# Kernel tuning notes

Hardware: AMD Instinct MI355X
Metric: run time of the kernel (lower is better)

## Reference

```python
import jax, jax.numpy as jnp
import numpy as np
import math

N = 4096; NFEAT = 512; HID = 128; H = 4; DH = HID // H; NC = 16; FF = 2 * HID


def _ln(x, g, b):
    m = jnp.mean(x, -1, keepdims=True)
    v = jnp.var(x, -1, keepdims=True)
    return (x - m) / jnp.sqrt(v + 1e-5) * g + b


def setup_inputs() -> dict:
    key = jax.random.key(0)
    ks = jax.random.split(key, 16)

    def w(k, shape):
        s = 1.0 / np.sqrt(shape[0])
        return jax.random.uniform(k, shape, jnp.float32, -s, s)

    inp = {}
    inp['e'] = jax.random.uniform(ks[0], (N,), jnp.float32, 0.0, 2.0)  # eigenvalues
    inp['u'] = jax.random.normal(ks[1], (N, N), jnp.float32) / np.sqrt(N)  # eigenvectors
    inp['x'] = jax.random.normal(ks[2], (N, NFEAT), jnp.float32)
    # feat_encoder: Linear(nfeat,hid) -> ReLU -> Linear(hid,nclass)
    inp['fe_w1'] = w(ks[3], (NFEAT, HID)); inp['fe_b1'] = jnp.zeros((HID,), jnp.float32)
    inp['fe_w2'] = w(ks[4], (HID, NC));    inp['fe_b2'] = jnp.zeros((NC,), jnp.float32)
    # eig_w: Linear(hid+1, hid)
    inp['ew_w'] = w(ks[5], (HID + 1, HID)); inp['ew_b'] = jnp.zeros((HID,), jnp.float32)
    inp['ln1_g'] = jnp.ones((HID,), jnp.float32); inp['ln1_b'] = jnp.zeros((HID,), jnp.float32)
    # custom MHA projections
    inp['wq'] = w(ks[6], (HID, HID)); inp['bq'] = jnp.zeros((HID,), jnp.float32)
    inp['wk'] = w(ks[7], (HID, HID)); inp['bk'] = jnp.zeros((HID,), jnp.float32)
    inp['wv'] = w(ks[8], (HID, HID)); inp['bv'] = jnp.zeros((HID,), jnp.float32)
    inp['wo'] = w(ks[9], (HID, HID)); inp['bo'] = jnp.zeros((HID,), jnp.float32)
    inp['ln2_g'] = jnp.ones((HID,), jnp.float32); inp['ln2_b'] = jnp.zeros((HID,), jnp.float32)
    # FFN with GELU
    inp['ffn_w1'] = w(ks[10], (HID, FF)); inp['ffn_b1'] = jnp.zeros((FF,), jnp.float32)
    inp['ffn_w2'] = w(ks[11], (FF, HID)); inp['ffn_b2'] = jnp.zeros((HID,), jnp.float32)
    # decoder: Linear(hid, nheads)
    inp['dec_w'] = w(ks[12], (HID, H)); inp['dec_b'] = jnp.zeros((H,), jnp.float32)
    # SpecLayer weight (norm='none' -> ones, [1, nheads+1, nclass])
    inp['spec_w'] = jnp.ones((1, H + 1, NC), jnp.float32)
    return inp


def reference(e, u, x, fe_w1, fe_b1, fe_w2, fe_b2, ew_w, ew_b, ln1_g, ln1_b,
              wq, bq, wk, bk, wv, bv, wo, bo, ln2_g, ln2_b,
              ffn_w1, ffn_b1, ffn_w2, ffn_b2, dec_w, dec_b, spec_w):
    n = e.shape[0]
    # feat_encoder (norm='none' path), dropout is identity at p=0
    h = jax.nn.relu(x @ fe_w1 + fe_b1) @ fe_w2 + fe_b2  # [N, NC]
    # SineEncoding
    div = jnp.exp(jnp.arange(0, HID, 2, dtype=jnp.float32) * (-math.log(10000.0) / HID))  # [HID/2]
    pe = (e * 100.0)[:, None] * div                     # [N, HID/2]
    sc = jnp.concatenate([jnp.sin(pe), jnp.cos(pe)], axis=1)   # [N, HID] (sin_cos_encoding)
    eeig = jnp.concatenate([e[:, None], sc], axis=1)           # [N, HID+1]
    eigw = eeig @ ew_w + ew_b                                  # [N, HID]
    # Custom multi-head attention with dot-product relative-position bias
    m = _ln(eigw, ln1_g, ln1_b)
    q = (m @ wq + bq).reshape(n, H, DH).transpose(1, 0, 2)     # [H, N, DH]
    k = (m @ wk + bk).reshape(n, H, DH).transpose(1, 0, 2)
    v = (m @ wv + bv).reshape(n, H, DH).transpose(1, 0, 2)
    rel = sc @ sc.T                                            # [N, N]
    scale = 1.0 / math.sqrt(DH)
    scores = jnp.einsum('hnd,hmd->hnm', q, k) * scale + rel[None] * scale  # [H, N, N]
    attn = jax.nn.softmax(scores, axis=-1)
    out = jnp.einsum('hnm,hmd->hnd', attn, v).transpose(1, 0, 2).reshape(n, HID)
    out = out @ wo + bo
    eig = eigw + out
    f = _ln(eig, ln2_g, ln2_b)
    f = jax.nn.gelu(f @ ffn_w1 + ffn_b1, approximate=False) @ ffn_w2 + ffn_b2
    eig = eig + f
    new_e = eig @ dec_w + dec_b                                # [N, H]
    # Spectral propagation (single SpecLayer, norm='none')
    utx = u.T @ h                                              # [N, NC]
    scaled = new_e.T[:, :, None] * utx[None]                   # [H, N, NC]
    props = jnp.einsum('nm,hmc->hnc', u, scaled)               # [H, N, NC]
    bf = jnp.concatenate([h[:, None, :], props.transpose(1, 0, 2)], axis=1)  # [N, H+1, NC]
    return jnp.sum(bf * spec_w, axis=1)                        # [N, NC]
```

## Files before the change

### kernel.cpp

```cpp
#include <hip/hip_runtime.h>
#include <math.h>

#define N 4096
#define NFEAT 512
#define HID 128
#define NHEAD 4
#define DH 32
#define NC 16
#define FF 256
#define NSPLIT 32
#define NCHUNK 8
#define CHUNKM (N / NCHUNK)
#define NGRP (CHUNKM / 128)

typedef _Float16 f16;
typedef unsigned int uint;
typedef _Float16 f16x8 __attribute__((ext_vector_type(8)));
typedef _Float16 f16x2 __attribute__((ext_vector_type(2)));
typedef float f32x16 __attribute__((ext_vector_type(16)));

#define SCALE 0.17677669529663687f
#define LOG2E 1.44269504088896f
#define SH2   (-14.0f * 1.44269504088896f)

__global__ __launch_bounds__(256) void k_feat(const float* __restrict__ x,
    const float* __restrict__ w1, const float* __restrict__ b1,
    const float* __restrict__ w2, const float* __restrict__ b2,
    float* __restrict__ h) {
  __shared__ float xs[8][NFEAT];
  __shared__ float h1s[8][HID];
  int r0 = blockIdx.x * 8, tid = threadIdx.x;
  for (int i = tid; i < 8 * (NFEAT / 4); i += 256) {
    int rr = i >> 7, c4 = i & 127;
    ((float4*)xs[rr])[c4] = *(const float4*)(x + (size_t)(r0 + rr) * NFEAT + c4 * 4);
  }
  __syncthreads();
  int c = tid & 127, rb = tid >> 7;
  float acc[4];
#pragma unroll
  for (int i = 0; i < 4; ++i) acc[i] = b1[c];
  for (int k2 = 0; k2 < NFEAT; ++k2) {
    float wv = w1[k2 * HID + c];
#pragma unroll
    for (int i = 0; i < 4; ++i) acc[i] += xs[rb + 2 * i][k2] * wv;
  }
#pragma unroll
  for (int i = 0; i < 4; ++i) h1s[rb + 2 * i][c] = fmaxf(acc[i], 0.f);
  __syncthreads();
  if (tid < 128) {
    int rr = tid >> 4, cc = tid & 15;
    float a2 = b2[cc];
    for (int k2 = 0; k2 < HID; ++k2)
      a2 += h1s[rr][k2] * w2[k2 * NC + cc];
    h[(size_t)(r0 + rr) * NC + cc] = a2;
  }
}

__global__ __launch_bounds__(256) void k_sine_eigw(const float* __restrict__ e,
    const float* __restrict__ eww, const float* __restrict__ ewb,
    f16* __restrict__ sc_h, f16* __restrict__ scS_h, float* __restrict__ eigw) {
  __shared__ float scs[8][HID];
  __shared__ float es[8];
  int r0 = blockIdx.x * 8, tid = threadIdx.x;
  if (tid < 8) es[tid] = e[r0 + tid];
  __syncthreads();
  for (int i = tid; i < 8 * 64; i += 256) {
    int rr = i >> 6, j = i & 63;
    float div = expf((float)(2 * j) * (-0.07195578415606394f));
    float pe = es[rr] * 100.0f * div;
    scs[rr][j]      = sinf(pe);
    scs[rr][j + 64] = cosf(pe);
  }
  __syncthreads();
  for (int i = tid; i < 8 * 64; i += 256) {
    int rr = i >> 6, jj = i & 63;
    float x0 = scs[rr][2 * jj], x1 = scs[rr][2 * jj + 1];
    f16x2 a; a[0] = (f16)x0; a[1] = (f16)x1;
    f16x2 b; b[0] = (f16)(x0 * SCALE); b[1] = (f16)(x1 * SCALE);
    ((f16x2*)sc_h)[(size_t)(r0 + rr) * 64 + jj] = a;
    ((f16x2*)scS_h)[(size_t)(r0 + rr) * 64 + jj] = b;
  }
  int c = tid & 127, rb = tid >> 7;
  float acc[4];
#pragma unroll
  for (int i = 0; i < 4; ++i) acc[i] = ewb[c] + es[rb + 2 * i] * eww[c];
  for (int k2 = 0; k2 < HID; ++k2) {
    float wv = eww[(1 + k2) * HID + c];
#pragma unroll
    for (int i = 0; i < 4; ++i) acc[i] += scs[rb + 2 * i][k2] * wv;
  }
#pragma unroll
  for (int i = 0; i < 4; ++i)
    eigw[(size_t)(r0 + rb + 2 * i) * HID + c] = acc[i];
}

__global__ __launch_bounds__(256) void k_ln(const float* __restrict__ in,
    const float* __restrict__ g, const float* __restrict__ b, float* __restrict__ out) {
  int row = blockIdx.x * 4 + (threadIdx.x >> 6);
  int l = threadIdx.x & 63;
  float2 v2 = *(const float2*)(in + (size_t)row * HID + l * 2);
  float s = v2.x + v2.y;
  float ss = v2.x * v2.x + v2.y * v2.y;
#pragma unroll
  for (int off = 32; off > 0; off >>= 1) {
    s  += __shfl_down(s, off, 64);
    ss += __shfl_down(ss, off, 64);
  }
  s = __shfl(s, 0, 64); ss = __shfl(ss, 0, 64);
  float mean = s * (1.0f / HID);
  float var = ss * (1.0f / HID) - mean * mean;
  float inv = 1.0f / sqrtf(var + 1e-5f);
  float2 g2 = *(const float2*)(g + l * 2);
  float2 b2 = *(const float2*)(b + l * 2);
  float2 o;
  o.x = (v2.x - mean) * inv * g2.x + b2.x;
  o.y = (v2.y - mean) * inv * g2.y + b2.y;
  *(float2*)(out + (size_t)row * HID + l * 2) = o;
}

template <bool RES, bool F16O>
__global__ __launch_bounds__(256) void k_lin128(const float* __restrict__ in,
    const float* __restrict__ w, const float* __restrict__ bias,
    const float* __restrict__ res, float* __restrict__ out, f16* __restrict__ outh,
    float oscale) {
  __shared__ float as[8][HID];
  int r0 = blockIdx.x * 8, tid = threadIdx.x;
  {
    int rr = tid >> 5, c4 = tid & 31;
    ((float4*)as[rr])[c4] = *(const float4*)(in + (size_t)(r0 + rr) * HID + c4 * 4);
  }
  __syncthreads();
  int c = tid & 127, rb = tid >> 7;
  float acc[4];
#pragma unroll
  for (int i = 0; i < 4; ++i) acc[i] = bias[c];
  for (int k2 = 0; k2 < HID; ++k2) {
    float wv = w[k2 * HID + c];
#pragma unroll
    for (int i = 0; i < 4; ++i) acc[i] += as[rb + 2 * i][k2] * wv;
  }
#pragma unroll
  for (int i = 0; i < 4; ++i) {
    int rr = rb + 2 * i;
    float o = acc[i];
    if (RES) o += res[(size_t)(r0 + rr) * HID + c];
    if (F16O) outh[(size_t)(r0 + rr) * HID + c] = (f16)(o * oscale);
    else      out[(size_t)(r0 + rr) * HID + c] = o;
  }
}

__global__ __launch_bounds__(256) void k_vT(const float* __restrict__ v, f16* __restrict__ vT) {
  int n0 = blockIdx.x * 64, d0 = blockIdx.y * 32, tid = threadIdx.x;
  int d = tid & 31;
#pragma unroll
  for (int it = 0; it < 4; ++it) {
    int j = (tid >> 5) + it * 8;
    float x0 = v[(size_t)(n0 + 2 * j) * HID + d0 + d];
    float x1 = v[(size_t)(n0 + 2 * j + 1) * HID + d0 + d];
    f16x2 hh; hh[0] = (f16)x0; hh[1] = (f16)x1;
    ((f16x2*)vT)[((size_t)(d0 + d) * N + n0) / 2 + j] = hh;
  }
}

__global__ __launch_bounds__(256, 4) void k_attn2(const f16* __restrict__ qh, const f16* __restrict__ kh,
    const f16* __restrict__ vTh, const f16* __restrict__ sch, const f16* __restrict__ scSh,
    float* __restrict__ pacc, float* __restrict__ pl) {
  __shared__ float relbuf[4 * 4 * 64 * 4];
  int tid = threadIdx.x, w = tid >> 6, lane = tid & 63, lrow = lane & 31, lhalf = lane >> 5;
  int n0 = blockIdx.x * 32, ntile = blockIdx.x, chunk = blockIdx.y;
  const f16* qp = qh + (size_t)(n0 + lrow) * HID + 32 * w + lhalf * 8;
  f16x8 qb0 = *(const f16x8*)(qp);
  f16x8 qb1 = *(const f16x8*)(qp + 16);
  f32x16 oacc = {0,0,0,0,0,0,0,0,0,0,0,0,0,0,0,0};
  float l = 0.f;
  for (int g = 0; g < NGRP; ++g) {
    int m0my = chunk * CHUNKM + (g * 4 + w) * 32;
    f32x16 rs = {0,0,0,0,0,0,0,0,0,0,0,0,0,0,0,0};
#pragma unroll
    for (int ks = 0; ks < 8; ++ks) {
      f16x8 as = *(const f16x8*)(scSh + (size_t)(m0my + lrow) * HID + ks * 16 + lhalf * 8);
      f16x8 bs = *(const f16x8*)(sch + (size_t)(n0 + lrow) * HID + ks * 16 + lhalf * 8);
      rs = __builtin_amdgcn_mfma_f32_32x32x16_f16(as, bs, rs, 0, 0, 0);
    }
    __syncthreads();
    {
      int base = w * 1024 + lane * 4;
      *(float4*)&relbuf[base +   0] = make_float4(rs[0],  rs[1],  rs[2],  rs[3]);
      *(float4*)&relbuf[base + 256] = make_float4(rs[4],  rs[5],  rs[6],  rs[7]);
      *(float4*)&relbuf[base + 512] = make_float4(rs[8],  rs[9],  rs[10], rs[11]);
      *(float4*)&relbuf[base + 768] = make_float4(rs[12], rs[13], rs[14], rs[15]);
    }
    __syncthreads();
#pragma unroll
    for (int t = 0; t < 4; ++t) {
      int m0 = chunk * CHUNKM + (g * 4 + t) * 32;
      f32x16 sacc;
      {
        int base = t * 1024 + lane * 4;
        float4 r0 = *(const float4*)&relbuf[base +   0];
        float4 r1 = *(const float4*)&relbuf[base + 256];
        float4 r2 = *(const float4*)&relbuf[base + 512];
        float4 r3 = *(const float4*)&relbuf[base + 768];
        sacc[0]=r0.x;  sacc[1]=r0.y;  sacc[2]=r0.z;  sacc[3]=r0.w;
        sacc[4]=r1.x;  sacc[5]=r1.y;  sacc[6]=r1.z;  sacc[7]=r1.w;
        sacc[8]=r2.x;  sacc[9]=r2.y;  sacc[10]=r2.z; sacc[11]=r2.w;
        sacc[12]=r3.x; sacc[13]=r3.y; sacc[14]=r3.z; sacc[15]=r3.w;
      }
      const f16* kp = kh + (size_t)(m0 + lrow) * HID + 32 * w + lhalf * 8;
      f16x8 ka0 = *(const f16x8*)(kp);
      f16x8 ka1 = *(const f16x8*)(kp + 16);
      const f16* vp = vTh + (size_t)(32 * w + lrow) * N + m0 + lhalf * 8;
      f16x8 va0 = *(const f16x8*)(vp);
      f16x8 va1 = *(const f16x8*)(vp + 16);
      sacc = __builtin_amdgcn_mfma_f32_32x32x16_f16(ka0, qb0, sacc, 0, 0, 0);
      sacc = __builtin_amdgcn_mfma_f32_32x32x16_f16(ka1, qb1, sacc, 0, 0, 0);
      uint w0[2], w1[2], w2[2], w3[2];
#pragma unroll
      for (int ks = 0; ks < 2; ++ks) {
        float p[8];
#pragma unroll
        for (int i = 0; i < 8; ++i)
          p[i] = exp2f(fmaf(sacc[ks * 8 + i], LOG2E, SH2));
        uint Wa = __builtin_bit_cast(uint, __builtin_amdgcn_cvt_pkrtz(p[0], p[1]));
        uint Wb = __builtin_bit_cast(uint, __builtin_amdgcn_cvt_pkrtz(p[2], p[3]));
        uint Wc = __builtin_bit_cast(uint, __builtin_amdgcn_cvt_pkrtz(p[4], p[5]));
        uint Wd = __builtin_bit_cast(uint, __builtin_amdgcn_cvt_pkrtz(p[6], p[7]));
        {
          f16x2 ha = __builtin_bit_cast(f16x2, Wa), hb = __builtin_bit_cast(f16x2, Wb);
          f16x2 hc = __builtin_bit_cast(f16x2, Wc), hd = __builtin_bit_cast(f16x2, Wd);
          l += (float)ha[0] + (float)ha[1] + (float)hb[0] + (float)hb[1]
             + (float)hc[0] + (float)hc[1] + (float)hd[0] + (float)hd[1];
        }
        uint Wax = (uint)__shfl_xor((int)Wa, 32, 64);
        uint Wbx = (uint)__shfl_xor((int)Wb, 32, 64);
        uint Wcx = (uint)__shfl_xor((int)Wc, 32, 64);
        uint Wdx = (uint)__shfl_xor((int)Wd, 32, 64);
        bool hi = (lhalf != 0);
        w0[ks] = hi ? Wcx : Wa;
        w1[ks] = hi ? Wdx : Wb;
        w2[ks] = hi ? Wc : Wax;
        w3[ks] = hi ? Wd : Wbx;
      }
      f16x8 pb0 = __builtin_bit_cast(f16x8, make_uint4(w0[0], w1[0], w2[0], w3[0]));
      f16x8 pb1 = __builtin_bit_cast(f16x8, make_uint4(w0[1], w1[1], w2[1], w3[1]));
      oacc = __builtin_amdgcn_mfma_f32_32x32x16_f16(va0, pb0, oacc, 0, 0, 0);
      oacc = __builtin_amdgcn_mfma_f32_32x32x16_f16(va1, pb1, oacc, 0, 0, 0);
    }
  }
  l += __shfl_xor(l, 32, 64);
  float* pp = pacc + ((size_t)(chunk * 4 + w) * 128 + ntile) * 1024 + lane * 16;
  *(float4*)(pp +  0) = make_float4(oacc[0],  oacc[1],  oacc[2],  oacc[3]);
  *(float4*)(pp +  4) = make_float4(oacc[4],  oacc[5],  oacc[6],  oacc[7]);
  *(float4*)(pp +  8) = make_float4(oacc[8],  oacc[9],  oacc[10], oacc[11]);
  *(float4*)(pp + 12) = make_float4(oacc[12], oacc[13], oacc[14], oacc[15]);
  if (lane < 32) pl[(size_t)(chunk * 4 + w) * N + n0 + lrow] = l;
}

__global__ __launch_bounds__(256) void k_attn_merge2(const float* __restrict__ pacc,
    const float* __restrict__ pl, float* __restrict__ attno) {
  __shared__ float ao[32][132];
  int tid = threadIdx.x, h = tid >> 6, lane = tid & 63, lrow = lane & 31, lhalf = lane >> 5;
  int ntile = blockIdx.x, n0 = ntile * 32;
  float o[16];
#pragma unroll
  for (int r = 0; r < 16; ++r) o[r] = 0.f;
  float l = 0.f;
#pragma unroll
  for (int c = 0; c < NCHUNK; ++c) {
    const float* pp = pacc + ((size_t)(c * 4 + h) * 128 + ntile) * 1024 + lane * 16;
    float4 r0 = *(const float4*)(pp), r1 = *(const float4*)(pp + 4);
    float4 r2 = *(const float4*)(pp + 8), r3 = *(const float4*)(pp + 12);
    o[0]+=r0.x; o[1]+=r0.y; o[2]+=r0.z; o[3]+=r0.w;
    o[4]+=r1.x; o[5]+=r1.y; o[6]+=r1.z; o[7]+=r1.w;
    o[8]+=r2.x; o[9]+=r2.y; o[10]+=r2.z; o[11]+=r2.w;
    o[12]+=r3.x; o[13]+=r3.y; o[14]+=r3.z; o[15]+=r3.w;
    l += pl[(size_t)(c * 4 + h) * N + n0 + lrow];
  }
  float inv = 1.0f / l;
#pragma unroll
  for (int r = 0; r < 16; ++r) {
    int d = (r & 3) + 8 * (r >> 2) + 4 * lhalf;
    ao[lrow][h * 32 + d] = o[r] * inv;
  }
  __syncthreads();
  for (int i = tid; i < 32 * 32; i += 256) {
    int row = i >> 5, c4 = i & 31;
    *(float4*)(attno + (size_t)(n0 + row) * HID + c4 * 4) = *(float4*)&ao[row][c4 * 4];
  }
}

__global__ __launch_bounds__(256) void k_ffn(const float* __restrict__ fln,
    const float* __restrict__ w1, const float* __restrict__ b1,
    const float* __restrict__ w2, const float* __restrict__ b2,
    const float* __restrict__ eig, float* __restrict__ out) {
  __shared__ float fs[8][HID];
  __shared__ float t1[8][FF];
  int r0 = blockIdx.x * 8, tid = threadIdx.x;
  {
    int rr = tid >> 5, c4 = tid & 31;
    ((float4*)fs[rr])[c4] = *(const float4*)(fln + (size_t)(r0 + rr) * HID + c4 * 4);
  }
  __syncthreads();
  {
    float acc[8];
#pragma unroll
    for (int i = 0; i < 8; ++i) acc[i] = b1[tid];
    for (int k2 = 0; k2 < HID; ++k2) {
      float wv = w1[k2 * FF + tid];
#pragma unroll
      for (int i = 0; i < 8; ++i) acc[i] += fs[i][k2] * wv;
    }
#pragma unroll
    for (int i = 0; i < 8; ++i) {
      float xg = acc[i];
      t1[i][tid] = 0.5f * xg * (1.0f + erff(xg * 0.7071067811865476f));
    }
  }
  __syncthreads();
  int c = tid & 127, rb = tid >> 7;
  float acc2[4];
#pragma unroll
  for (int i = 0; i < 4; ++i) acc2[i] = b2[c];
  for (int k2 = 0; k2 < FF; ++k2) {
    float wv = w2[k2 * HID + c];
#pragma unroll
    for (int i = 0; i < 4; ++i) acc2[i] += t1[rb + 2 * i][k2] * wv;
  }
#pragma unroll
  for (int i = 0; i < 4; ++i) {
    int rr = r0 + rb + 2 * i;
    out[(size_t)rr * HID + c] = acc2[i] + eig[(size_t)rr * HID + c];
  }
}

__global__ __launch_bounds__(256) void k_dec(const float* __restrict__ eig2,
    const float* __restrict__ dw, const float* __restrict__ db, float* __restrict__ newe) {
  int tid = threadIdx.x;
  int r = tid >> 4, j = (tid >> 2) & 3, q = tid & 3;
  int n = blockIdx.x * 16 + r;
  const float* ep = eig2 + (size_t)n * HID + q * 32;
  float a = 0.f;
#pragma unroll
  for (int t4 = 0; t4 < 8; ++t4) {
    float4 e4 = *(const float4*)(ep + t4 * 4);
    int k0 = q * 32 + t4 * 4;
    a += e4.x * dw[k0 * NHEAD + j] + e4.y * dw[(k0 + 1) * NHEAD + j]
       + e4.z * dw[(k0 + 2) * NHEAD + j] + e4.w * dw[(k0 + 3) * NHEAD + j];
  }
  a += __shfl_down(a, 1, 64);
  a += __shfl_down(a, 2, 64);
  if (q == 0) newe[n * NHEAD + j] = db[j] + a;
}

__global__ __launch_bounds__(256) void k_utx(const float* __restrict__ u,
    const float* __restrict__ h, float* __restrict__ putx) {
  __shared__ float hs[128][NC];
  int tid = threadIdx.x;
  int m = blockIdx.x * 256 + tid;
  int n0 = blockIdx.y * 128;
  for (int i = tid; i < 128 * 4; i += 256) {
    int row = i >> 2, cq = i & 3;
    ((float4*)hs[row])[cq] = *(const float4*)(h + (size_t)(n0 + row) * NC + cq * 4);
  }
  __syncthreads();
  float acc[16];
#pragma unroll
  for (int c = 0; c < 16; ++c) acc[c] = 0.f;
  for (int nb = 0; nb < 16; ++nb) {
    float uv[8];
#pragma unroll
    for (int t = 0; t < 8; ++t)
      uv[t] = u[(size_t)(n0 + nb * 8 + t) * N + m];
#pragma unroll
    for (int t = 0; t < 8; ++t) {
      int nl = nb * 8 + t;
      float4 h0 = ((const float4*)hs[nl])[0];
      float4 h1 = ((const float4*)hs[nl])[1];
      float4 h2 = ((const float4*)hs[nl])[2];
      float4 h3 = ((const float4*)hs[nl])[3];
      acc[0]  += uv[t] * h0.x;  acc[1]  += uv[t] * h0.y;
      acc[2]  += uv[t] * h0.z;  acc[3]  += uv[t] * h0.w;
      acc[4]  += uv[t] * h1.x;  acc[5]  += uv[t] * h1.y;
      acc[6]  += uv[t] * h1.z;  acc[7]  += uv[t] * h1.w;
      acc[8]  += uv[t] * h2.x;  acc[9]  += uv[t] * h2.y;
      acc[10] += uv[t] * h2.z;  acc[11] += uv[t] * h2.w;
      acc[12] += uv[t] * h3.x;  acc[13] += uv[t] * h3.y;
      acc[14] += uv[t] * h3.z;  acc[15] += uv[t] * h3.w;
    }
  }
  float* o = putx + ((size_t)blockIdx.y * N + m) * NC;
  *(float4*)(o +  0) = make_float4(acc[0],  acc[1],  acc[2],  acc[3]);
  *(float4*)(o +  4) = make_float4(acc[4],  acc[5],  acc[6],  acc[7]);
  *(float4*)(o +  8) = make_float4(acc[8],  acc[9],  acc[10], acc[11]);
  *(float4*)(o + 12) = make_float4(acc[12], acc[13], acc[14], acc[15]);
}

__global__ __launch_bounds__(256) void k_sbuild(const float* __restrict__ putx,
    const float* __restrict__ newe, const float* __restrict__ specw,
    float* __restrict__ sT) {
  int i = blockIdx.x * 256 + threadIdx.x;
  int m = i >> 2, cq = i & 3;
  float4 t = make_float4(0.f, 0.f, 0.f, 0.f);
#pragma unroll 8
  for (int ch = 0; ch < NSPLIT; ++ch) {
    float4 p = *(const float4*)(putx + ((size_t)ch * N + m) * NC + cq * 4);
    t.x += p.x; t.y += p.y; t.z += p.z; t.w += p.w;
  }
  float4 ne = *(const float4*)(newe + (size_t)m * NHEAD);
  float fac[4];
#pragma unroll
  for (int cc = 0; cc < 4; ++cc) {
    int c = cq * 4 + cc;
    fac[cc] = ne.x * specw[1 * NC + c] + ne.y * specw[2 * NC + c]
            + ne.z * specw[3 * NC + c] + ne.w * specw[4 * NC + c];
  }
  sT[(size_t)(cq * 4 + 0) * N + m] = t.x * fac[0];
  sT[(size_t)(cq * 4 + 1) * N + m] = t.y * fac[1];
  sT[(size_t)(cq * 4 + 2) * N + m] = t.z * fac[2];
  sT[(size_t)(cq * 4 + 3) * N + m] = t.w * fac[3];
}

__global__ __launch_bounds__(256) void k_final(const float* __restrict__ u,
    const float* __restrict__ sT, float* __restrict__ pfin) {
  __shared__ float sTl[16][256];
  int tid = threadIdx.x, w = tid >> 6, lane = tid & 63;
  int r0 = blockIdx.x * 16;
  size_t mbase = (size_t)blockIdx.y * 2048;
  float a[4][16];
#pragma unroll
  for (int r = 0; r < 4; ++r)
#pragma unroll
    for (int c = 0; c < 16; ++c) a[r][c] = 0.f;
  for (int chunk = 0; chunk < 8; ++chunk) {
    size_t mc0 = mbase + chunk * 256;
    __syncthreads();
    for (int i = tid; i < 16 * 64; i += 256) {
      int c = i >> 6, q = i & 63;
      ((float4*)&sTl[c][0])[q] = *(const float4*)(sT + (size_t)c * N + mc0 + q * 4);
    }
    __syncthreads();
    float4 u4[4];
#pragma unroll
    for (int r = 0; r < 4; ++r)
      u4[r] = *(const float4*)(u + (size_t)(r0 + w * 4 + r) * N + mc0 + 4 * lane);
#pragma unroll
    for (int c = 0; c < 16; ++c) {
      float4 sv = *(const float4*)&sTl[c][4 * lane];
#pragma unroll
      for (int r = 0; r < 4; ++r)
        a[r][c] += u4[r].x * sv.x + u4[r].y * sv.y + u4[r].z * sv.z + u4[r].w * sv.w;
    }
  }
#pragma unroll
  for (int off = 32; off > 0; off >>= 1)
#pragma unroll
    for (int r = 0; r < 4; ++r)
#pragma unroll
      for (int c = 0; c < 16; ++c)
        a[r][c] += __shfl_xor(a[r][c], off, 64);
  if (lane == 0) {
#pragma unroll
    for (int r = 0; r < 4; ++r) {
      float* op = pfin + ((size_t)blockIdx.y * N + r0 + w * 4 + r) * NC;
      *(float4*)(op +  0) = make_float4(a[r][0],  a[r][1],  a[r][2],  a[r][3]);
      *(float4*)(op +  4) = make_float4(a[r][4],  a[r][5],  a[r][6],  a[r][7]);
      *(float4*)(op +  8) = make_float4(a[r][8],  a[r][9],  a[r][10], a[r][11]);
      *(float4*)(op + 12) = make_float4(a[r][12], a[r][13], a[r][14], a[r][15]);
    }
  }
}

__global__ __launch_bounds__(256) void k_finmerge(const float* __restrict__ pfin,
    const float* __restrict__ h, const float* __restrict__ specw, float* __restrict__ out) {
  int i = blockIdx.x * 256 + threadIdx.x;
  int n = i >> 2, cq = i & 3;
  float4 f0 = *(const float4*)(pfin + (size_t)n * NC + cq * 4);
  float4 f1 = *(const float4*)(pfin + ((size_t)N + n) * NC + cq * 4);
  float4 h4 = *(const float4*)(h + (size_t)n * NC + cq * 4);
  int c0 = cq * 4;
  float4 o;
  o.x = f0.x + f1.x + h4.x * specw[c0 + 0];
  o.y = f0.y + f1.y + h4.y * specw[c0 + 1];
  o.z = f0.z + f1.z + h4.z * specw[c0 + 2];
  o.w = f0.w + f1.w + h4.w * specw[c0 + 3];
  *(float4*)(out + (size_t)n * NC + cq * 4) = o;
}

extern "C" void kernel_launch(void* const* d_in, const int* in_sizes, int n_in,
                              void* d_out, int out_size, void* d_ws, size_t ws_size,
                              hipStream_t stream) {
  const float* e    = (const float*)d_in[0];
  const float* u    = (const float*)d_in[1];
  const float* x    = (const float*)d_in[2];
  const float* few1 = (const float*)d_in[3];
  const float* feb1 = (const float*)d_in[4];
  const float* few2 = (const float*)d_in[5];
  const float* feb2 = (const float*)d_in[6];
  const float* eww  = (const float*)d_in[7];
  const float* ewb  = (const float*)d_in[8];
  const float* ln1g = (const float*)d_in[9];
  const float* ln1b = (const float*)d_in[10];
  const float* wq   = (const float*)d_in[11];
  const float* bq   = (const float*)d_in[12];
  const float* wk   = (const float*)d_in[13];
  const float* bk   = (const float*)d_in[14];
  const float* wv_  = (const float*)d_in[15];
  const float* bv   = (const float*)d_in[16];
  const float* wo   = (const float*)d_in[17];
  const float* bo   = (const float*)d_in[18];
  const float* ln2g = (const float*)d_in[19];
  const float* ln2b = (const float*)d_in[20];
  const float* fw1  = (const float*)d_in[21];
  const float* fb1  = (const float*)d_in[22];
  const float* fw2  = (const float*)d_in[23];
  const float* fb2  = (const float*)d_in[24];
  const float* dw   = (const float*)d_in[25];
  const float* db   = (const float*)d_in[26];
  const float* spw  = (const float*)d_in[27];
  float* out = (float*)d_out;

  char* wsb = (char*)d_ws;
  auto alloc = [&](size_t bytes) { char* p = wsb; wsb += (bytes + 1023) & ~(size_t)1023; return p; };
  float* h    = (float*)alloc(N * NC * 4);
  f16*  sc_h  = (f16*)alloc(N * HID * 2);
  f16*  scS_h = (f16*)alloc(N * HID * 2);
  float* eigw = (float*)alloc(N * HID * 4);
  float* mln  = (float*)alloc(N * HID * 4);
  f16*  q_h   = (f16*)alloc(N * HID * 2);
  f16*  k_h   = (f16*)alloc(N * HID * 2);
  float* v    = (float*)alloc(N * HID * 4);
  f16*  vT_h  = (f16*)alloc(N * HID * 2);
  float* attno= (float*)alloc(N * HID * 4);
  float* eig  = (float*)alloc(N * HID * 4);
  float* fln  = (float*)alloc(N * HID * 4);
  float* eig2 = (float*)alloc(N * HID * 4);
  float* newe = (float*)alloc(N * NHEAD * 4);
  float* sT   = (float*)alloc((size_t)NC * N * 4);
  float* putx = (float*)alloc((size_t)NSPLIT * N * NC * 4);
  float* pacc = (float*)alloc((size_t)NCHUNK * 4 * 128 * 1024 * 4);
  float* pl   = (float*)alloc((size_t)NCHUNK * 4 * N * 4);
  float* pfin = (float*)alloc((size_t)2 * N * NC * 4);

  k_feat<<<N / 8, 256, 0, stream>>>(x, few1, feb1, few2, feb2, h);
  k_utx<<<dim3(N / 256, NSPLIT), 256, 0, stream>>>(u, h, putx);
  k_sine_eigw<<<N / 8, 256, 0, stream>>>(e, eww, ewb, sc_h, scS_h, eigw);
  k_ln<<<N / 4, 256, 0, stream>>>(eigw, ln1g, ln1b, mln);
  k_lin128<false, true><<<N / 8, 256, 0, stream>>>(mln, wq, bq, nullptr, nullptr, q_h, SCALE);
  k_lin128<false, true><<<N / 8, 256, 0, stream>>>(mln, wk, bk, nullptr, nullptr, k_h, 1.0f);
  k_lin128<false, false><<<N / 8, 256, 0, stream>>>(mln, wv_, bv, nullptr, v, nullptr, 1.0f);
  k_vT<<<dim3(N / 64, 4), 256, 0, stream>>>(v, vT_h);
  k_attn2<<<dim3(128, NCHUNK), 256, 0, stream>>>(q_h, k_h, vT_h, sc_h, scS_h, pacc, pl);
  k_attn_merge2<<<128, 256, 0, stream>>>(pacc, pl, attno);
  k_lin128<true, false><<<N / 8, 256, 0, stream>>>(attno, wo, bo, eigw, eig, nullptr, 1.0f);
  k_ln<<<N / 4, 256, 0, stream>>>(eig, ln2g, ln2b, fln);
  k_ffn<<<N / 8, 256, 0, stream>>>(fln, fw1, fb1, fw2, fb2, eig, eig2);
  k_dec<<<N / 16, 256, 0, stream>>>(eig2, dw, db, newe);
  k_sbuild<<<N * 4 / 256, 256, 0, stream>>>(putx, newe, spw, sT);
  k_final<<<dim3(N / 16, 2), 256, 0, stream>>>(u, sT, pfin);
  k_finmerge<<<N * 4 / 256, 256, 0, stream>>>(pfin, h, spw, out);
}
```

Measured before the change: 378.0 us.

## Fuse LayerNorm with QKV projections and split attention into more chunks

Replaces the separate LayerNorm kernel and three linear-projection launches with one kernel that normalizes each row in shared memory and computes Q, K and V together, removing the intermediate buffer and three launches. The attention kernel now splits the key dimension into twice as many chunks and requests higher occupancy, so more blocks run concurrently at the cost of more partial results for the merge step. Inside attention, the softmax denominator is summed in fp32 before conversion to f16, and where available a lane-32 permute swap replaces four cross-half shuffles. The occupancy hint may force register spills, and the larger partial buffer adds merge traffic; the merge kernel must also handle the new chunk count.

```diff
diff --git a/kernel.cpp b/kernel.cpp
--- a/kernel.cpp
+++ b/kernel.cpp
@@ -9,7 +9,7 @@
 #define NC 16
 #define FF 256
 #define NSPLIT 32
-#define NCHUNK 8
+#define NCHUNK 16
 #define CHUNKM (N / NCHUNK)
 #define NGRP (CHUNKM / 128)
 
@@ -18,6 +18,7 @@
 typedef _Float16 f16x8 __attribute__((ext_vector_type(8)));
 typedef _Float16 f16x2 __attribute__((ext_vector_type(2)));
 typedef float f32x16 __attribute__((ext_vector_type(16)));
+typedef uint uint2v __attribute__((ext_vector_type(2)));
 
 #define SCALE 0.17677669529663687f
 #define LOG2E 1.44269504088896f
@@ -118,6 +119,60 @@
   *(float2*)(out + (size_t)row * HID + l * 2) = o;
 }
 
+__global__ __launch_bounds__(256) void k_lnqkv(const float* __restrict__ eigw,
+    const float* __restrict__ g, const float* __restrict__ b,
+    const float* __restrict__ wq, const float* __restrict__ bq,
+    const float* __restrict__ wk, const float* __restrict__ bk,
+    const float* __restrict__ wv, const float* __restrict__ bv,
+    f16* __restrict__ qh, f16* __restrict__ kh, float* __restrict__ v) {
+  __shared__ float as[8][HID];
+  int r0 = blockIdx.x * 8, tid = threadIdx.x;
+  {
+    int rr = tid >> 5, ln = tid & 31;
+    float4 x4 = *(const float4*)(eigw + (size_t)(r0 + rr) * HID + ln * 4);
+    float s = x4.x + x4.y + x4.z + x4.w;
+    float ss = x4.x * x4.x + x4.y * x4.y + x4.z * x4.z + x4.w * x4.w;
+#pragma unroll
+    for (int off = 16; off > 0; off >>= 1) {
+      s  += __shfl_xor(s, off, 32);
+      ss += __shfl_xor(ss, off, 32);
+    }
+    float mean = s * (1.0f / HID);
+    float var = ss * (1.0f / HID) - mean * mean;
+    float inv = 1.0f / sqrtf(var + 1e-5f);
+    float4 g4 = *(const float4*)(g + ln * 4);
+    float4 b4 = *(const float4*)(b + ln * 4);
+    float4 o;
+    o.x = (x4.x - mean) * inv * g4.x + b4.x;
+    o.y = (x4.y - mean) * inv * g4.y + b4.y;
+    o.z = (x4.z - mean) * inv * g4.z + b4.z;
+    o.w = (x4.w - mean) * inv * g4.w + b4.w;
+    *(float4*)&as[rr][ln * 4] = o;
+  }
+  __syncthreads();
+  int c = tid & 127, rb = tid >> 7;
+  float aq[4], ak[4], av[4];
+#pragma unroll
+  for (int i = 0; i < 4; ++i) { aq[i] = bq[c]; ak[i] = bk[c]; av[i] = bv[c]; }
+  for (int k2 = 0; k2 < HID; ++k2) {
+    float wqv = wq[k2 * HID + c];
+    float wkv = wk[k2 * HID + c];
+    float wvv = wv[k2 * HID + c];
+#pragma unroll
+    for (int i = 0; i < 4; ++i) {
+      float xv = as[rb + 2 * i][k2];
+      aq[i] += xv * wqv; ak[i] += xv * wkv; av[i] += xv * wvv;
+    }
+  }
+#pragma unroll
+  for (int i = 0; i < 4; ++i) {
+    int rr = r0 + rb + 2 * i;
+    qh[(size_t)rr * HID + c] = (f16)(aq[i] * SCALE);
+    kh[(size_t)rr * HID + c] = (f16)ak[i];
+    v[(size_t)rr * HID + c]  = av[i];
+  }
+}
+
 template <bool RES, bool F16O>
 __global__ __launch_bounds__(256) void k_lin128(const float* __restrict__ in,
     const float* __restrict__ w, const float* __restrict__ bias,
@@ -162,7 +217,7 @@
   }
 }
 
-__global__ __launch_bounds__(256, 4) void k_attn2(const f16* __restrict__ qh, const f16* __restrict__ kh,
+__global__ __launch_bounds__(256, 8) void k_attn2(const f16* __restrict__ qh, const f16* __restrict__ kh,
     const f16* __restrict__ vTh, const f16* __restrict__ sch, const f16* __restrict__ scSh,
     float* __restrict__ pacc, float* __restrict__ pl) {
   __shared__ float relbuf[4 * 4 * 64 * 4];
@@ -221,16 +276,17 @@
 #pragma unroll
         for (int i = 0; i < 8; ++i)
           p[i] = exp2f(fmaf(sacc[ks * 8 + i], LOG2E, SH2));
+        l += ((p[0] + p[1]) + (p[2] + p[3])) + ((p[4] + p[5]) + (p[6] + p[7]));
         uint Wa = __builtin_bit_cast(uint, __builtin_amdgcn_cvt_pkrtz(p[0], p[1]));
         uint Wb = __builtin_bit_cast(uint, __builtin_amdgcn_cvt_pkrtz(p[2], p[3]));
         uint Wc = __builtin_bit_cast(uint, __builtin_amdgcn_cvt_pkrtz(p[4], p[5]));
         uint Wd = __builtin_bit_cast(uint, __builtin_amdgcn_cvt_pkrtz(p[6], p[7]));
-        {
-          f16x2 ha = __builtin_bit_cast(f16x2, Wa), hb = __builtin_bit_cast(f16x2, Wb);
-          f16x2 hc = __builtin_bit_cast(f16x2, Wc), hd = __builtin_bit_cast(f16x2, Wd);
-          l += (float)ha[0] + (float)ha[1] + (float)hb[0] + (float)hb[1]
-             + (float)hc[0] + (float)hc[1] + (float)hd[0] + (float)hd[1];
-        }
+#if __has_builtin(__builtin_amdgcn_permlane32_swap)
+        uint2v r02 = __builtin_amdgcn_permlane32_swap(Wa, Wc, false, false);
+        uint2v r13 = __builtin_amdgcn_permlane32_swap(Wb, Wd, false, false);
+        w0[ks] = r02[0]; w2[ks] = r02[1];
+        w1[ks] = r13[0]; w3[ks] = r13[1];
+#else
         uint Wax = (uint)__shfl_xor((int)Wa, 32, 64);
         uint Wbx = (uint)__shfl_xor((int)Wb, 32, 64);
         uint Wcx = (uint)__shfl_xor((int)Wc, 32, 64);
@@ -240,6 +296,7 @@
         w1[ks] = hi ? Wdx : Wb;
         w2[ks] = hi ? Wc : Wax;
         w3[ks] = hi ? Wd : Wbx;
+#endif
       }
       f16x8 pb0 = __builtin_bit_cast(f16x8, make_uint4(w0[0], w1[0], w2[0], w3[0]));
       f16x8 pb1 = __builtin_bit_cast(f16x8, make_uint4(w0[1], w1[1], w2[1], w3[1]));
@@ -525,7 +582,6 @@
   f16*  sc_h  = (f16*)alloc(N * HID * 2);
   f16*  scS_h = (f16*)alloc(N * HID * 2);
   float* eigw = (float*)alloc(N * HID * 4);
-  float* mln  = (float*)alloc(N * HID * 4);
   f16*  q_h   = (f16*)alloc(N * HID * 2);
   f16*  k_h   = (f16*)alloc(N * HID * 2);
   float* v    = (float*)alloc(N * HID * 4);
@@ -544,10 +600,7 @@
   k_feat<<<N / 8, 256, 0, stream>>>(x, few1, feb1, few2, feb2, h);
   k_utx<<<dim3(N / 256, NSPLIT), 256, 0, stream>>>(u, h, putx);
   k_sine_eigw<<<N / 8, 256, 0, stream>>>(e, eww, ewb, sc_h, scS_h, eigw);
-  k_ln<<<N / 4, 256, 0, stream>>>(eigw, ln1g, ln1b, mln);
-  k_lin128<false, true><<<N / 8, 256, 0, stream>>>(mln, wq, bq, nullptr, nullptr, q_h, SCALE);
-  k_lin128<false, true><<<N / 8, 256, 0, stream>>>(mln, wk, bk, nullptr, nullptr, k_h, 1.0f);
-  k_lin128<false, false><<<N / 8, 256, 0, stream>>>(mln, wv_, bv, nullptr, v, nullptr, 1.0f);
+  k_lnqkv<<<N / 8, 256, 0, stream>>>(eigw, ln1g, ln1b, wq, bq, wk, bk, wv_, bv, q_h, k_h, v);
   k_vT<<<dim3(N / 64, 4), 256, 0, stream>>>(v, vT_h);
   k_attn2<<<dim3(128, NCHUNK), 256, 0, stream>>>(q_h, k_h, vT_h, sc_h, scS_h, pacc, pl);
   k_attn_merge2<<<128, 256, 0, stream>>>(pacc, pl, attno);
```

Result: slower. 492.5 us (+30.3%).
